# Optimization experiments

Measured on AMD Instinct MI355X. Metric: run time of the kernel, lower is better.

## Reference

```python
import jax, jax.numpy as jnp
import numpy as np

B, IN_DIM, H1, H2, HID, SPEC_H, OUT, E = 16384, 1024, 2048, 2048, 1024, 2048, 1, 8


def setup_inputs() -> dict:
    key = jax.random.key(0)
    ks = jax.random.split(key, 12)

    def lin(k, fan_in, shape):
        # torch nn.Linear default init: U(-1/sqrt(fan_in), 1/sqrt(fan_in))
        bound = 1.0 / np.sqrt(fan_in)
        return jax.random.uniform(k, shape, jnp.float32, -bound, bound)

    return {
        "x": jax.random.normal(ks[0], (B, IN_DIM), jnp.float32),
        "d": jax.random.randint(ks[1], (B,), 0, E, jnp.int64),
        # shared encoder: Linear(IN,H1)+ReLU, Linear(H1,H2)+ReLU, Linear(H2,HID)
        "enc_W0": lin(ks[2], IN_DIM, (IN_DIM, H1)),
        "enc_b0": lin(ks[3], IN_DIM, (H1,)),
        "enc_W1": lin(ks[4], H1, (H1, H2)),
        "enc_b1": lin(ks[5], H1, (H2,)),
        "enc_W2": lin(ks[6], H2, (H2, HID)),
        "enc_b2": lin(ks[7], H2, (HID,)),
        # per-domain heads: Linear(HID,SPEC_H)+ReLU, Linear(SPEC_H,OUT)
        "spec_W1": lin(ks[8], HID, (E, HID, SPEC_H)),
        "spec_b1": lin(ks[9], HID, (E, SPEC_H)),
        "spec_W2": lin(ks[10], SPEC_H, (E, SPEC_H, OUT)),
        "spec_b2": lin(ks[11], SPEC_H, (E, OUT)),
    }


def reference(x, d, enc_W0, enc_b0, enc_W1, enc_b1, enc_W2, enc_b2,
              spec_W1, spec_b1, spec_W2, spec_b2):
    # Shared encoder (dropout is identity in eval mode)
    z = jax.nn.relu(x @ enc_W0 + enc_b0)        # [B, H1]
    z = jax.nn.relu(z @ enc_W1 + enc_b1)        # [B, H2]
    z = z @ enc_W2 + enc_b2                     # [B, HID]

    # Domain-routed heads: compute each expert on the full batch, combine by mask.
    n_experts = spec_W1.shape[0]
    out = jnp.zeros((z.shape[0], spec_W2.shape[-1]), dtype=z.dtype)  # [B, OUT]
    for e in range(n_experts):
        h = jax.nn.relu(z @ spec_W1[e] + spec_b1[e])  # [B, SPEC_H]
        y = h @ spec_W2[e] + spec_b2[e]               # [B, OUT]
        out = out + jnp.where((d == e)[:, None], y, jnp.zeros_like(y))
    return out
```

## Files before the change

kernel.cpp:

```cpp
#include <hip/hip_runtime.h>
#include <hip/hip_bf16.h>
#include <stdint.h>

#define B_SZ   16384
#define IN_DIM 1024
#define H1     2048
#define H2     2048
#define HID    1024
#define SPEC_H 2048
#define NE     8
#define MAX_TILES 136

typedef __bf16 bf16x8 __attribute__((ext_vector_type(8)));
typedef float  f32x4  __attribute__((ext_vector_type(4)));
typedef ushort us8    __attribute__((ext_vector_type(8)));

__device__ __forceinline__ ushort f2bf(float f) {
  uint32_t u = __float_as_uint(f);
  u += 0x7FFF + ((u >> 16) & 1);
  return (ushort)(u >> 16);
}

__device__ __forceinline__ void gl_lds16(const void* g, void* l) {
  __builtin_amdgcn_global_load_lds(
      (const __attribute__((address_space(1))) void*)g,
      (__attribute__((address_space(3))) void*)l, 16, 0, 0);
}


struct TransDesc { const float* src; ushort* dst; int K, N, nx, base; };

struct PrepArgs {
  TransDesc td[4];
  const float* x; ushort* xb;
  const int* d; int* counts; const float* sb2; float* out;
  int castBase;
  int cntBase;
};

__global__ void prep_all(PrepArgs pa) {
  int g = blockIdx.x;
  int t = threadIdx.x;
  if (g >= pa.cntBase) {
    __shared__ int hist[NE];
    if (t < NE) hist[t] = 0;
    __syncthreads();
    int i = (g - pa.cntBase) * 256 + t;
    int e = pa.d[i];
    atomicAdd(&hist[e], 1);
    pa.out[i] = pa.sb2[e];
    __syncthreads();
    if (t < NE) atomicAdd(&pa.counts[t], hist[t]);
    return;
  }
  if (g >= pa.castBase) {
    size_t i = (size_t)(g - pa.castBase) * 4096 + (size_t)t * 16;
    float4 v0 = *(const float4*)(pa.x + i);
    float4 v1 = *(const float4*)(pa.x + i + 4);
    float4 v2 = *(const float4*)(pa.x + i + 8);
    float4 v3 = *(const float4*)(pa.x + i + 12);
    uint32_t p0 = f2bf(v0.x) | ((uint32_t)f2bf(v0.y) << 16);
    uint32_t p1 = f2bf(v0.z) | ((uint32_t)f2bf(v0.w) << 16);
    uint32_t p2 = f2bf(v1.x) | ((uint32_t)f2bf(v1.y) << 16);
    uint32_t p3 = f2bf(v1.z) | ((uint32_t)f2bf(v1.w) << 16);
    uint32_t p4 = f2bf(v2.x) | ((uint32_t)f2bf(v2.y) << 16);
    uint32_t p5 = f2bf(v2.z) | ((uint32_t)f2bf(v2.w) << 16);
    uint32_t p6 = f2bf(v3.x) | ((uint32_t)f2bf(v3.y) << 16);
    uint32_t p7 = f2bf(v3.z) | ((uint32_t)f2bf(v3.w) << 16);
    int4 pkA = {(int)p0, (int)p1, (int)p2, (int)p3};
    int4 pkB = {(int)p4, (int)p5, (int)p6, (int)p7};
    *(int4*)(pa.xb + i) = pkA;
    *(int4*)(pa.xb + i + 8) = pkB;
    return;
  }
  __shared__ float tile[64][65];
  int wsel = 0;
#pragma unroll
  for (int i = 1; i < 4; ++i)
    if (g >= pa.td[i].base) wsel = i;
  TransDesc dd = pa.td[wsel];
  int local = g - dd.base;
  int per = dd.nx * (dd.K >> 6);
  int z = local / per;
  int r = local - z * per;
  int bx = r % dd.nx, by = r / dd.nx;
  int n0 = bx * 64, k0 = by * 64;
  const float* src = dd.src + (size_t)z * dd.K * dd.N;
  ushort* dst = dd.dst + (size_t)z * dd.K * dd.N;
  int lk = t >> 4;
  int ln4 = (t & 15) * 4;
#pragma unroll
  for (int j = 0; j < 4; ++j) {
    int k = lk + j * 16;
    float4 v = *(const float4*)(src + (size_t)(k0 + k) * dd.N + n0 + ln4);
    tile[ln4 + 0][k] = v.x;
    tile[ln4 + 1][k] = v.y;
    tile[ln4 + 2][k] = v.z;
    tile[ln4 + 3][k] = v.w;
  }
  __syncthreads();
  int kc = (t & 7) * 8;
  int nb = t >> 3;
#pragma unroll
  for (int j = 0; j < 2; ++j) {
    int nn = nb + j * 32;
    us8 o;
#pragma unroll
    for (int q = 0; q < 8; ++q) o[q] = f2bf(tile[nn][kc + q]);
    *(us8*)(dst + (size_t)(n0 + nn) * dd.K + k0 + kc) = o;
  }
}


__global__ void build_k(const int* __restrict__ counts, int* __restrict__ catalog,
                        int* __restrict__ poff, int* __restrict__ cursors) {
  if (threadIdx.x == 0) {
    int off = 0;
    for (int e = 0; e < NE; ++e) {
      poff[e] = off * 128;
      int nt = (counts[e] + 127) >> 7;
      for (int i = 0; i < nt; ++i) catalog[off + i] = e;
      off += nt;
      cursors[e] = 0;
    }
    for (int i = off; i < MAX_TILES; ++i) catalog[i] = -1;
  }
}

__global__ void scatter_k(const int* __restrict__ d, const int* __restrict__ poff,
                          int* __restrict__ cursors, int* __restrict__ perm) {
  __shared__ int wcnt[4][NE];
  __shared__ int basee[NE];
  int t = threadIdx.x;
  int i = blockIdx.x * 256 + t;
  int e = d[i];
  int w = t >> 6, lane = t & 63;
  uint64_t mymask = 0;
#pragma unroll
  for (int ee = 0; ee < NE; ++ee) {
    uint64_t mm = __ballot(e == ee);
    if (lane == 0) wcnt[w][ee] = __popcll(mm);
    if (e == ee) mymask = mm;
  }
  int rank = __popcll(mymask & ((1ull << lane) - 1ull));
  __syncthreads();
  if (t < NE) {
    int s = 0;
#pragma unroll
    for (int ww = 0; ww < 4; ++ww) { int c = wcnt[ww][t]; wcnt[ww][t] = s; s += c; }
    basee[t] = atomicAdd(&cursors[t], s);
  }
  __syncthreads();
  int pos = basee[e] + wcnt[w][e] + rank;
  perm[poff[e] + pos] = i;
}


template <int RELU>
__global__ __launch_bounds__(512, 2) void gemm8(
    const ushort* __restrict__ A, const ushort* __restrict__ Bt,
    const float* __restrict__ bias, ushort* __restrict__ C,
    int M, int N, int K, int lognx) {
  __shared__ __align__(16) ushort sm[65536];
  const int t = threadIdx.x;
  const int h = blockIdx.x;
  const int g = h >> 3;
  const int nx = 1 << lognx;
  const int by = (h & 7) + ((g >> lognx) << 3);
  const int bx = g & (nx - 1);
  const int m0 = by * 256, n0 = bx * 256;
  const int w = t >> 6, lane = t & 63;
  const int wm = (w >> 2) * 128, wn = (w & 3) * 64;
  const int q = lane >> 4, rl = lane & 15;
  const int row_s = t >> 3, pch_s = t & 7;
  const int NT = K >> 6;

  f32x4 acc[8][4];
#pragma unroll
  for (int mi = 0; mi < 8; ++mi)
#pragma unroll
    for (int ni = 0; ni < 4; ++ni) acc[mi][ni] = 0.0f;

  bf16x8 afr[4][2], bfr[4][2];

  auto STG = [&](int tt, int which) {
    if (tt >= NT) return;
    const int c = tt & 1;
    const int k0 = tt << 6;
    if (which >= 2) {
      const int R0 = (which - 2) << 7;
#pragma unroll
      for (int j = 0; j < 2; ++j) {
        int row = (j << 6) + row_s;
        int gch = pch_s ^ (row & 7);
        gl_lds16(A + (size_t)(m0 + R0 + row) * K + k0 + (gch << 3),
                 sm + (c << 15) + (R0 << 6) + (j << 12) + (w << 9));
      }
    } else {
      const int R0 = which << 7;
#pragma unroll
      for (int j = 0; j < 2; ++j) {
        int row = (j << 6) + row_s;
        int gch = pch_s ^ (row & 7);
        gl_lds16(Bt + (size_t)(n0 + R0 + row) * K + k0 + (gch << 3),
                 sm + (c << 15) + 16384 + (R0 << 6) + (j << 12) + (w << 9));
      }
    }
  };

  STG(0, 0); STG(0, 1); STG(0, 2); STG(0, 3);
  asm volatile("s_waitcnt vmcnt(4)" ::: "memory");
  STG(1, 0); STG(1, 1); STG(1, 2);
  asm volatile("s_waitcnt vmcnt(6)" ::: "memory");
  __builtin_amdgcn_s_barrier();

  for (int tt = 0; tt < NT; ++tt) {
    const ushort* bufA = sm + ((tt & 1) << 15);
    const ushort* bufB = bufA + 16384;

#pragma unroll
    for (int mi = 0; mi < 4; ++mi)
#pragma unroll
      for (int kk = 0; kk < 2; ++kk) {
        int pc = ((kk << 2) + q) ^ (rl & 7);
        afr[mi][kk] = __builtin_bit_cast(bf16x8,
            *(const int4*)(bufA + (wm + (mi << 4) + rl) * 64 + (pc << 3)));
      }
#pragma unroll
    for (int ni = 0; ni < 4; ++ni)
#pragma unroll
      for (int kk = 0; kk < 2; ++kk) {
        int pc = ((kk << 2) + q) ^ (rl & 7);
        bfr[ni][kk] = __builtin_bit_cast(bf16x8,
            *(const int4*)(bufB + (wn + (ni << 4) + rl) * 64 + (pc << 3)));
      }
    asm volatile("" ::: "memory");
    __builtin_amdgcn_sched_barrier(0);
    STG(tt + 1, 3);
    __builtin_amdgcn_s_barrier();
    asm volatile("s_waitcnt lgkmcnt(0)" ::: "memory");
    __builtin_amdgcn_sched_barrier(0);
    __builtin_amdgcn_s_setprio(1);
#pragma unroll
    for (int kk = 0; kk < 2; ++kk)
#pragma unroll
      for (int mi = 0; mi < 4; ++mi)
#pragma unroll
        for (int ni = 0; ni < 2; ++ni)
          acc[mi][ni] = __builtin_amdgcn_mfma_f32_16x16x32_bf16(
              afr[mi][kk], bfr[ni][kk], acc[mi][ni], 0, 0, 0);
    __builtin_amdgcn_s_setprio(0);
    __builtin_amdgcn_s_barrier();

    STG(tt + 2, 0);
    __builtin_amdgcn_s_barrier();
    __builtin_amdgcn_s_setprio(1);
#pragma unroll
    for (int kk = 0; kk < 2; ++kk)
#pragma unroll
      for (int mi = 0; mi < 4; ++mi)
#pragma unroll
        for (int ni = 2; ni < 4; ++ni)
          acc[mi][ni] = __builtin_amdgcn_mfma_f32_16x16x32_bf16(
              afr[mi][kk], bfr[ni][kk], acc[mi][ni], 0, 0, 0);
    __builtin_amdgcn_s_setprio(0);
    __builtin_amdgcn_s_barrier();

#pragma unroll
    for (int mi = 0; mi < 4; ++mi)
#pragma unroll
      for (int kk = 0; kk < 2; ++kk) {
        int pc = ((kk << 2) + q) ^ (rl & 7);
        afr[mi][kk] = __builtin_bit_cast(bf16x8,
            *(const int4*)(bufA + (wm + ((mi + 4) << 4) + rl) * 64 + (pc << 3)));
      }
    asm volatile("" ::: "memory");
    __builtin_amdgcn_sched_barrier(0);
    STG(tt + 2, 1);
    __builtin_amdgcn_s_barrier();
    asm volatile("s_waitcnt lgkmcnt(0)" ::: "memory");
    __builtin_amdgcn_sched_barrier(0);
    __builtin_amdgcn_s_setprio(1);
#pragma unroll
    for (int kk = 0; kk < 2; ++kk)
#pragma unroll
      for (int mi = 0; mi < 4; ++mi)
#pragma unroll
        for (int ni = 0; ni < 2; ++ni)
          acc[mi + 4][ni] = __builtin_amdgcn_mfma_f32_16x16x32_bf16(
              afr[mi][kk], bfr[ni][kk], acc[mi + 4][ni], 0, 0, 0);
    __builtin_amdgcn_s_setprio(0);
    __builtin_amdgcn_s_barrier();

    STG(tt + 2, 2);
    if (tt + 2 < NT)      asm volatile("s_waitcnt vmcnt(6)" ::: "memory");
    else if (tt + 1 < NT) asm volatile("s_waitcnt vmcnt(0)" ::: "memory");
    __builtin_amdgcn_s_barrier();
    __builtin_amdgcn_s_setprio(1);
#pragma unroll
    for (int kk = 0; kk < 2; ++kk)
#pragma unroll
      for (int mi = 0; mi < 4; ++mi)
#pragma unroll
        for (int ni = 2; ni < 4; ++ni)
          acc[mi + 4][ni] = __builtin_amdgcn_mfma_f32_16x16x32_bf16(
              afr[mi][kk], bfr[ni][kk], acc[mi + 4][ni], 0, 0, 0);
    __builtin_amdgcn_s_setprio(0);
    __builtin_amdgcn_s_barrier();
  }

  float bv[4];
#pragma unroll
  for (int ni = 0; ni < 4; ++ni) bv[ni] = bias[n0 + wn + ni * 16 + rl];
#pragma unroll
  for (int mi = 0; mi < 8; ++mi) {
    int rg = m0 + wm + mi * 16 + q * 4;
#pragma unroll
    for (int r = 0; r < 4; ++r) {
#pragma unroll
      for (int ni = 0; ni < 4; ++ni) {
        float v = acc[mi][ni][r] + bv[ni];
        if (RELU) v = fmaxf(v, 0.0f);
        C[(size_t)(rg + r) * N + n0 + wn + ni * 16 + rl] = f2bf(v);
      }
    }
  }
}


__global__ __launch_bounds__(256, 2) void expert_fused(
    const ushort* __restrict__ Z, const ushort* __restrict__ W1t,
    const float* __restrict__ b1, const float* __restrict__ w2,
    const int* __restrict__ perm, const int* __restrict__ catalog,
    const int* __restrict__ poff, const int* __restrict__ counts,
    float* __restrict__ out) {
  const int id = blockIdx.x;
  const int tile = (id & 7) * 17 + ((id >> 3) >> 4);
  const int ycol = (id >> 3) & 15;
  int e = catalog[tile];
  if (e < 0) return;
  __shared__ __align__(16) ushort lA[128 * 64];
  __shared__ __align__(16) ushort lB[128 * 64];
  __shared__ int perml[128];
  __shared__ float ysum[128];
  const int t = threadIdx.x;
  if (t < 128) {
    int slot = tile * 128 + t;
    int rel = slot - poff[e];
    perml[t] = (rel < counts[e]) ? perm[slot] : -1;
    ysum[t] = 0.0f;
  }
  __syncthreads();

  const int n0 = ycol * 128;
  const ushort* Bt = W1t + (size_t)e * SPEC_H * HID;
  const float* b1e = b1 + (size_t)e * SPEC_H;
  const float* w2e = w2 + (size_t)e * SPEC_H;
  const int w = t >> 6, lane = t & 63;
  const int wm = (w >> 1) * 64, wn = (w & 1) * 64;
  const int q = lane >> 4, rl = lane & 15;

  f32x4 acc[4][4];
#pragma unroll
  for (int mi = 0; mi < 4; ++mi)
#pragma unroll
    for (int ni = 0; ni < 4; ++ni) acc[mi][ni] = 0.0f;

  const int row_s = t >> 3;
  const int pch_s = t & 7;

  for (int k0 = 0; k0 < HID; k0 += 64) {
    __syncthreads();
#pragma unroll
    for (int j = 0; j < 4; ++j) {
      int row = j * 32 + row_s;
      int gch = pch_s ^ (row & 7);
      int zr = perml[row];
      zr = zr < 0 ? 0 : zr;
      gl_lds16(Z + (size_t)zr * HID + k0 + gch * 8, lA + j * 2048 + w * 512);
      gl_lds16(Bt + (size_t)(n0 + row) * HID + k0 + gch * 8, lB + j * 2048 + w * 512);
    }
    __syncthreads();
#pragma unroll
    for (int kk = 0; kk < 2; ++kk) {
      bf16x8 af[4], bfr[4];
#pragma unroll
      for (int i = 0; i < 4; ++i) {
        int pc = (kk * 4 + q) ^ (rl & 7);
        af[i]  = __builtin_bit_cast(bf16x8, *(const int4*)(lA + (wm + i * 16 + rl) * 64 + pc * 8));
        bfr[i] = __builtin_bit_cast(bf16x8, *(const int4*)(lB + (wn + i * 16 + rl) * 64 + pc * 8));
      }
#pragma unroll
      for (int mi = 0; mi < 4; ++mi)
#pragma unroll
        for (int ni = 0; ni < 4; ++ni)
          acc[mi][ni] = __builtin_amdgcn_mfma_f32_16x16x32_bf16(af[mi], bfr[ni], acc[mi][ni], 0, 0, 0);
    }
  }

  float w2v[4], b1v[4];
#pragma unroll
  for (int ni = 0; ni < 4; ++ni) {
    int n = n0 + wn + ni * 16 + rl;
    w2v[ni] = w2e[n];
    b1v[ni] = b1e[n];
  }
#pragma unroll
  for (int mi = 0; mi < 4; ++mi) {
#pragma unroll
    for (int r = 0; r < 4; ++r) {
      float p = 0.0f;
#pragma unroll
      for (int ni = 0; ni < 4; ++ni) {
        float h = acc[mi][ni][r] + b1v[ni];
        h = fmaxf(h, 0.0f);
        p += h * w2v[ni];
      }
      p += __shfl_xor(p, 1);
      p += __shfl_xor(p, 2);
      p += __shfl_xor(p, 4);
      p += __shfl_xor(p, 8);
      if (rl == 0) atomicAdd(&ysum[wm + mi * 16 + q * 4 + r], p);
    }
  }
  __syncthreads();
  if (t < 128) {
    int orow = perml[t];
    if (orow >= 0) atomicAdd(&out[orow], ysum[t]);
  }
}


extern "C" void kernel_launch(void* const* d_in, const int* in_sizes, int n_in,
                              void* d_out, int out_size, void* d_ws, size_t ws_size,
                              hipStream_t stream) {
  const float* x   = (const float*)d_in[0];
  const int*   d   = (const int*)d_in[1];
  const float* eW0 = (const float*)d_in[2];
  const float* eb0 = (const float*)d_in[3];
  const float* eW1 = (const float*)d_in[4];
  const float* eb1 = (const float*)d_in[5];
  const float* eW2 = (const float*)d_in[6];
  const float* eb2 = (const float*)d_in[7];
  const float* sW1 = (const float*)d_in[8];
  const float* sb1 = (const float*)d_in[9];
  const float* sW2 = (const float*)d_in[10];
  const float* sb2 = (const float*)d_in[11];
  float* out = (float*)d_out;

  const size_t fixed = ((size_t)(4 + 8 + 4 + 32 + 32 + 32) << 20) + (1 << 20);
  int CH = 8192;
  if (ws_size >= fixed + (size_t)16384 * 8192) CH = 16384;

  char* p = (char*)d_ws;
  ushort* W0t  = (ushort*)p; p += (size_t)IN_DIM * H1 * 2;
  ushort* W1t  = (ushort*)p; p += (size_t)H1 * H2 * 2;
  ushort* W2t  = (ushort*)p; p += (size_t)H2 * HID * 2;
  ushort* sW1t = (ushort*)p; p += (size_t)NE * HID * SPEC_H * 2;
  ushort* Zb   = (ushort*)p; p += (size_t)B_SZ * HID * 2;
  ushort* xb   = (ushort*)p; p += (size_t)B_SZ * IN_DIM * 2;
  int* counts  = (int*)p; p += 64;
  int* cursors = (int*)p; p += 64;
  int* poff    = (int*)p; p += 64;
  int* catalog = (int*)p; p += 1024;
  int* perm    = (int*)p; p += (size_t)MAX_TILES * 128 * 4;
  p = (char*)(((uintptr_t)p + 255) & ~(uintptr_t)255);
  ushort* z1 = (ushort*)p; p += (size_t)CH * H1 * 2;
  ushort* z2 = (ushort*)p; p += (size_t)CH * H2 * 2;

  hipMemsetAsync(counts, 0, 64, stream);

  PrepArgs pa;
  pa.td[0] = {eW0, W0t, IN_DIM, H1, H1 / 64, 0};
  pa.td[1] = {eW1, W1t, H1, H2, H2 / 64, 512};
  pa.td[2] = {eW2, W2t, H2, HID, HID / 64, 1536};
  pa.td[3] = {sW1, sW1t, HID, SPEC_H, SPEC_H / 64, 2048};
  pa.x = x; pa.xb = xb;
  pa.d = d; pa.counts = counts; pa.sb2 = sb2; pa.out = out;
  pa.castBase = 6144;
  pa.cntBase = 6144 + 4096;
  prep_all<<<6144 + 4096 + 64, 256, 0, stream>>>(pa);

  build_k<<<1, 64, 0, stream>>>(counts, catalog, poff, cursors);
  scatter_k<<<B_SZ / 256, 256, 0, stream>>>(d, poff, cursors, perm);

  for (int c = 0; c < B_SZ; c += CH) {
    gemm8<1><<<(CH / 256) * (H1 / 256), 512, 0, stream>>>(
        xb + (size_t)c * IN_DIM, W0t, eb0, z1, CH, H1, IN_DIM, 3);
    gemm8<1><<<(CH / 256) * (H2 / 256), 512, 0, stream>>>(
        z1, W1t, eb1, z2, CH, H2, H1, 3);
    gemm8<0><<<(CH / 256) * (HID / 256), 512, 0, stream>>>(
        z2, W2t, eb2, Zb + (size_t)c * HID, CH, HID, H2, 2);
  }

  expert_fused<<<MAX_TILES * 16, 256, 0, stream>>>(
      Zb, sW1t, sb1, sW2, perm, catalog, poff, counts, out);
}
```

Before: 570.1 us.

## Reorder GEMM quadrant schedule to interleave LDS fragment loads with MFMA phases

Splits the A and B register fragments into low and high halves and reorders the four MFMA quadrant phases (LL, LH, HH, HL). Each phase now loads only the fragments it newly needs, so LDS reads are spread across phases instead of front-loaded. An early partial lgkmcnt wait and removal of one prologue vmcnt wait aim to overlap shared-memory reads with global-to-LDS staging and compute. Register use rises slightly, since both A halves and both B halves are live at once. Correctness depends on the revised waitcnt values matching the outstanding loads.

```diff
diff --git a/kernel.cpp b/kernel.cpp
--- a/kernel.cpp
+++ b/kernel.cpp
@@ -181,7 +181,7 @@
 #pragma unroll
     for (int ni = 0; ni < 4; ++ni) acc[mi][ni] = 0.0f;
 
-  bf16x8 afr[4][2], bfr[4][2];
+  bf16x8 aL[4][2], aH[4][2], bL[2][2], bH[2][2];
 
   auto STG = [&](int tt, int which) {
     if (tt >= NT) return;
@@ -209,7 +209,6 @@
   };
 
   STG(0, 0); STG(0, 1); STG(0, 2); STG(0, 3);
-  asm volatile("s_waitcnt vmcnt(4)" ::: "memory");
   STG(1, 0); STG(1, 1); STG(1, 2);
   asm volatile("s_waitcnt vmcnt(6)" ::: "memory");
   __builtin_amdgcn_s_barrier();
@@ -223,19 +222,18 @@
 #pragma unroll
       for (int kk = 0; kk < 2; ++kk) {
         int pc = ((kk << 2) + q) ^ (rl & 7);
-        afr[mi][kk] = __builtin_bit_cast(bf16x8,
+        aL[mi][kk] = __builtin_bit_cast(bf16x8,
             *(const int4*)(bufA + (wm + (mi << 4) + rl) * 64 + (pc << 3)));
       }
 #pragma unroll
-    for (int ni = 0; ni < 4; ++ni)
+    for (int ni = 0; ni < 2; ++ni)
 #pragma unroll
       for (int kk = 0; kk < 2; ++kk) {
         int pc = ((kk << 2) + q) ^ (rl & 7);
-        bfr[ni][kk] = __builtin_bit_cast(bf16x8,
+        bL[ni][kk] = __builtin_bit_cast(bf16x8,
             *(const int4*)(bufB + (wn + (ni << 4) + rl) * 64 + (pc << 3)));
       }
-    asm volatile("" ::: "memory");
-    __builtin_amdgcn_sched_barrier(0);
+    asm volatile("s_waitcnt lgkmcnt(8)" ::: "memory");
     STG(tt + 1, 3);
     __builtin_amdgcn_s_barrier();
     asm volatile("s_waitcnt lgkmcnt(0)" ::: "memory");
@@ -248,35 +246,19 @@
 #pragma unroll
         for (int ni = 0; ni < 2; ++ni)
           acc[mi][ni] = __builtin_amdgcn_mfma_f32_16x16x32_bf16(
-              afr[mi][kk], bfr[ni][kk], acc[mi][ni], 0, 0, 0);
+              aL[mi][kk], bL[ni][kk], acc[mi][ni], 0, 0, 0);
     __builtin_amdgcn_s_setprio(0);
     __builtin_amdgcn_s_barrier();
 
-    STG(tt + 2, 0);
-    __builtin_amdgcn_s_barrier();
-    __builtin_amdgcn_s_setprio(1);
-#pragma unroll
-    for (int kk = 0; kk < 2; ++kk)
-#pragma unroll
-      for (int mi = 0; mi < 4; ++mi)
-#pragma unroll
-        for (int ni = 2; ni < 4; ++ni)
-          acc[mi][ni] = __builtin_amdgcn_mfma_f32_16x16x32_bf16(
-              afr[mi][kk], bfr[ni][kk], acc[mi][ni], 0, 0, 0);
-    __builtin_amdgcn_s_setprio(0);
-    __builtin_amdgcn_s_barrier();
-
-#pragma unroll
-    for (int mi = 0; mi < 4; ++mi)
+#pragma unroll
+    for (int ni = 0; ni < 2; ++ni)
 #pragma unroll
       for (int kk = 0; kk < 2; ++kk) {
         int pc = ((kk << 2) + q) ^ (rl & 7);
-        afr[mi][kk] = __builtin_bit_cast(bf16x8,
-            *(const int4*)(bufA + (wm + ((mi + 4) << 4) + rl) * 64 + (pc << 3)));
-      }
-    asm volatile("" ::: "memory");
-    __builtin_amdgcn_sched_barrier(0);
-    STG(tt + 2, 1);
+        bH[ni][kk] = __builtin_bit_cast(bf16x8,
+            *(const int4*)(bufB + (wn + ((ni + 2) << 4) + rl) * 64 + (pc << 3)));
+      }
+    STG(tt + 2, 0);
     __builtin_amdgcn_s_barrier();
     asm volatile("s_waitcnt lgkmcnt(0)" ::: "memory");
     __builtin_amdgcn_sched_barrier(0);
@@ -287,8 +269,32 @@
       for (int mi = 0; mi < 4; ++mi)
 #pragma unroll
         for (int ni = 0; ni < 2; ++ni)
-          acc[mi + 4][ni] = __builtin_amdgcn_mfma_f32_16x16x32_bf16(
-              afr[mi][kk], bfr[ni][kk], acc[mi + 4][ni], 0, 0, 0);
+          acc[mi][ni + 2] = __builtin_amdgcn_mfma_f32_16x16x32_bf16(
+              aL[mi][kk], bH[ni][kk], acc[mi][ni + 2], 0, 0, 0);
+    __builtin_amdgcn_s_setprio(0);
+    __builtin_amdgcn_s_barrier();
+
+#pragma unroll
+    for (int mi = 0; mi < 4; ++mi)
+#pragma unroll
+      for (int kk = 0; kk < 2; ++kk) {
+        int pc = ((kk << 2) + q) ^ (rl & 7);
+        aH[mi][kk] = __builtin_bit_cast(bf16x8,
+            *(const int4*)(bufA + (wm + ((mi + 4) << 4) + rl) * 64 + (pc << 3)));
+      }
+    STG(tt + 2, 1);
+    __builtin_amdgcn_s_barrier();
+    asm volatile("s_waitcnt lgkmcnt(0)" ::: "memory");
+    __builtin_amdgcn_sched_barrier(0);
+    __builtin_amdgcn_s_setprio(1);
+#pragma unroll
+    for (int kk = 0; kk < 2; ++kk)
+#pragma unroll
+      for (int mi = 0; mi < 4; ++mi)
+#pragma unroll
+        for (int ni = 0; ni < 2; ++ni)
+          acc[mi + 4][ni + 2] = __builtin_amdgcn_mfma_f32_16x16x32_bf16(
+              aH[mi][kk], bH[ni][kk], acc[mi + 4][ni + 2], 0, 0, 0);
     __builtin_amdgcn_s_setprio(0);
     __builtin_amdgcn_s_barrier();
 
@@ -302,9 +308,9 @@
 #pragma unroll
       for (int mi = 0; mi < 4; ++mi)
 #pragma unroll
-        for (int ni = 2; ni < 4; ++ni)
+        for (int ni = 0; ni < 2; ++ni)
           acc[mi + 4][ni] = __builtin_amdgcn_mfma_f32_16x16x32_bf16(
-              afr[mi][kk], bfr[ni][kk], acc[mi + 4][ni], 0, 0, 0);
+              aH[mi][kk], bL[ni][kk], acc[mi + 4][ni], 0, 0, 0);
     __builtin_amdgcn_s_setprio(0);
     __builtin_amdgcn_s_barrier();
   }
```

After: 564.5 us. No clear change (-1.0%).
